# Performance work log

Hardware: AMD Instinct MI355X
Metric: run time of the kernel (lower is better)

Reference implementation:

```python
import jax, jax.numpy as jnp
import numpy as np

EPS = 1e-8  # LayerNorm eps from __init__
B, C1, T, H, AUX, OUT = 4, 512, 256, 64, 256, 512


def prelu(x, a):
    # torch nn.PReLU with num_parameters=1 (scalar slope, init 0.25)
    return jnp.where(x >= 0, x, a * x)


def layernorm(x, w, b):
    mu = jnp.mean(x, axis=-1, keepdims=True)
    var = jnp.mean(jnp.square(x - mu), axis=-1, keepdims=True)
    return (x - mu) * jax.lax.rsqrt(var + EPS) * w + b


def setup_inputs() -> dict:
    key = jax.random.key(0)
    k0, k1, k2, k3 = jax.random.split(key, 4)
    x = jax.random.normal(k0, (B, C1, T, H), dtype=jnp.float32)
    s = jax.random.normal(k1, (B, AUX), dtype=jnp.float32)
    # pre: PReLU + LayerNorm(input_dim)
    prelu1_a = jnp.full((), 0.25, dtype=jnp.float32)
    ln1_w = jnp.ones((C1,), dtype=jnp.float32)
    ln1_b = jnp.zeros((C1,), dtype=jnp.float32)
    # post: Linear(input_dim+aux_dim, output_dim) + PReLU + LayerNorm(output_dim)
    lim = 1.0 / np.sqrt(C1 + AUX)
    W = jax.random.uniform(k2, (OUT, C1 + AUX), jnp.float32, -lim, lim)
    b = jax.random.uniform(k3, (OUT,), jnp.float32, -lim, lim)
    prelu2_a = jnp.full((), 0.25, dtype=jnp.float32)
    ln2_w = jnp.ones((OUT,), dtype=jnp.float32)
    ln2_b = jnp.zeros((OUT,), dtype=jnp.float32)
    return {"x": x, "s": s, "prelu1_a": prelu1_a, "ln1_w": ln1_w, "ln1_b": ln1_b,
            "W": W, "b": b, "prelu2_a": prelu2_a, "ln2_w": ln2_w, "ln2_b": ln2_b}


def reference(x, s, prelu1_a, ln1_w, ln1_b, W, b, prelu2_a, ln2_w, ln2_b):
    Bb, C, Tt, Hh = x.shape
    xt = jnp.transpose(x, (0, 2, 3, 1))  # b c t h -> b t h c
    # NOTE: source computes pre(x) into y but then overwrites y with the concat,
    # so this branch is dead code; reproduced for fidelity (DCE'd under jit).
    _pre = layernorm(prelu(xt, prelu1_a), ln1_w, ln1_b)
    # speaker embedding broadcast over (t, h), concatenated on channel axis
    s4 = jnp.broadcast_to(s[:, None, None, :], (Bb, Tt, Hh, s.shape[-1]))
    cat = jnp.concatenate([xt, s4], axis=-1)            # (b, t, h, c1+aux)
    z = jnp.einsum('bthc,oc->btho', cat, W) + b          # Linear
    z = layernorm(prelu(z, prelu2_a), ln2_w, ln2_b)      # PReLU + LayerNorm
    y = xt + z                                           # residual add
    return jnp.transpose(y, (0, 3, 1, 2))                # b t h c -> b c t h
```

## Files before the change

### kernel.cpp

```cpp
#include <hip/hip_runtime.h>
#include <hip/hip_bf16.h>

#define B_   4
#define C1_  512
#define T_   256
#define H_   64
#define TH_  (T_*H_)
#define AUX_ 256
#define OUT_ 512
#define INF_ 768
#define BK   32
#define THB  64
#define WSTR 40

typedef __attribute__((ext_vector_type(8))) short bf16x8;
typedef __attribute__((ext_vector_type(4))) float f32x4;

__device__ __forceinline__ ushort bf16u(float f) {
    __hip_bfloat16 h = __float2bfloat16(f);
    return *reinterpret_cast<ushort*>(&h);
}

__global__ void wconv_kernel(const float* __restrict__ W, ushort* __restrict__ Wbf) {
    int idx = (blockIdx.x * 256 + threadIdx.x) * 4;
    int o = idx >> 9, c = idx & 511;
    const float4 v = *(const float4*)(W + (size_t)o * INF_ + c);
    ushort4 u = make_ushort4(bf16u(v.x), bf16u(v.y), bf16u(v.z), bf16u(v.w));
    *(ushort4*)(Wbf + idx) = u;
}

__global__ void sw_kernel(const float* __restrict__ s, const float* __restrict__ W,
                          const float* __restrict__ bias, float* __restrict__ sW) {
    __shared__ float sl[AUX_];
    int b = blockIdx.x, o = threadIdx.x;
    for (int c = threadIdx.x; c < AUX_; c += 512) sl[c] = s[b * AUX_ + c];
    __syncthreads();
    float acc = bias[o];
    const float* wr = W + (size_t)o * INF_ + C1_;
    #pragma unroll 8
    for (int c = 0; c < AUX_; c += 4) {
        float4 w = *(const float4*)(wr + c);
        acc += sl[c] * w.x + sl[c+1] * w.y + sl[c+2] * w.z + sl[c+3] * w.w;
    }
    sW[b * OUT_ + o] = acc;
}

__global__ __launch_bounds__(512) void fused_kernel(
    const float* __restrict__ X, const ushort* __restrict__ Wbf,
    const float* __restrict__ sW, const float* __restrict__ a2p,
    const float* __restrict__ ln2w, const float* __restrict__ ln2b,
    float* __restrict__ Yout)
{
    __shared__ __align__(16) ushort Ws[C1_ * WSTR];
    __shared__ __align__(16) ushort Xs[THB * WSTR];
    __shared__ float red[8][THB][2];

    const int tid  = threadIdx.x;
    const int lane = tid & 63;
    const int w    = tid >> 6;
    const int b    = blockIdx.y;
    const int th0  = blockIdx.x * THB;
    const float* xb = X + (size_t)b * C1_ * TH_;

    const int l15 = lane & 15;
    const int lhi = lane >> 4;

    f32x4 acc[4][4] = {};

    for (int kk = 0; kk < C1_ / BK; ++kk) {
        const int kc = kk * BK;
        #pragma unroll
        for (int it = 0; it < 4; ++it) {
            int slot = tid + it * 512;
            int r = slot >> 2, q = slot & 3;
            const uint4 v = *(const uint4*)(Wbf + (size_t)r * C1_ + kc + q * 8);
            *(uint4*)(&Ws[r * WSTR + q * 8]) = v;
        }
        {
            int i = tid >> 4, j4 = tid & 15;
            const float4 v = *(const float4*)(xb + (size_t)(kc + i) * TH_ + th0 + j4 * 4);
            Xs[(j4 * 4 + 0) * WSTR + i] = bf16u(v.x);
            Xs[(j4 * 4 + 1) * WSTR + i] = bf16u(v.y);
            Xs[(j4 * 4 + 2) * WSTR + i] = bf16u(v.z);
            Xs[(j4 * 4 + 3) * WSTR + i] = bf16u(v.w);
        }
        __syncthreads();
        bf16x8 af[4], bfr[4];
        #pragma unroll
        for (int fm = 0; fm < 4; ++fm)
            af[fm] = *(const bf16x8*)(&Ws[(w * 64 + fm * 16 + l15) * WSTR + lhi * 8]);
        #pragma unroll
        for (int fn = 0; fn < 4; ++fn)
            bfr[fn] = *(const bf16x8*)(&Xs[(fn * 16 + l15) * WSTR + lhi * 8]);
        #pragma unroll
        for (int fm = 0; fm < 4; ++fm) {
            #pragma unroll
            for (int fn = 0; fn < 4; ++fn)
                acc[fm][fn] = __builtin_amdgcn_mfma_f32_16x16x32_bf16(
                    af[fm], bfr[fn], acc[fm][fn], 0, 0, 0);
        }
        __syncthreads();
    }

    const float a2 = a2p[0];
    const int obase = w * 64;
    float swv[4][4];
    #pragma unroll
    for (int fm = 0; fm < 4; ++fm)
        #pragma unroll
        for (int r = 0; r < 4; ++r)
            swv[fm][r] = sW[b * OUT_ + obase + fm * 16 + lhi * 4 + r];

    float s1[4] = {0,0,0,0}, s2[4] = {0,0,0,0};
    #pragma unroll
    for (int fm = 0; fm < 4; ++fm) {
        #pragma unroll
        for (int fn = 0; fn < 4; ++fn) {
            #pragma unroll
            for (int r = 0; r < 4; ++r) {
                float z = acc[fm][fn][r] + swv[fm][r];
                float v = z >= 0.f ? z : a2 * z;
                acc[fm][fn][r] = v;
                s1[fn] += v; s2[fn] += v * v;
            }
        }
    }
    #pragma unroll
    for (int fn = 0; fn < 4; ++fn) {
        s1[fn] += __shfl_xor(s1[fn], 16, 64);
        s2[fn] += __shfl_xor(s2[fn], 16, 64);
        s1[fn] += __shfl_xor(s1[fn], 32, 64);
        s2[fn] += __shfl_xor(s2[fn], 32, 64);
    }
    if (lane < 16) {
        #pragma unroll
        for (int fn = 0; fn < 4; ++fn) {
            red[w][fn * 16 + lane][0] = s1[fn];
            red[w][fn * 16 + lane][1] = s2[fn];
        }
    }
    __syncthreads();
    float mean[4], rstd[4];
    #pragma unroll
    for (int fn = 0; fn < 4; ++fn) {
        float t1 = 0.f, t2 = 0.f;
        #pragma unroll
        for (int ww = 0; ww < 8; ++ww) {
            t1 += red[ww][fn * 16 + l15][0];
            t2 += red[ww][fn * 16 + l15][1];
        }
        float mu = t1 * (1.0f / OUT_);
        mean[fn] = mu;
        float var = t2 * (1.0f / OUT_) - mu * mu;
        rstd[fn] = rsqrtf(var + 1e-8f);
    }
    #pragma unroll
    for (int fm = 0; fm < 4; ++fm) {
        #pragma unroll
        for (int r = 0; r < 4; ++r) {
            int o = obase + fm * 16 + lhi * 4 + r;
            float wo = ln2w[o], bo = ln2b[o];
            const float* xrow = xb + (size_t)o * TH_ + th0;
            float* yrow = Yout + ((size_t)b * OUT_ + o) * TH_ + th0;
            #pragma unroll
            for (int fn = 0; fn < 4; ++fn) {
                int col = fn * 16 + l15;
                float resid = xrow[col];
                yrow[col] = resid + (acc[fm][fn][r] - mean[fn]) * rstd[fn] * wo + bo;
            }
        }
    }
}

extern "C" void kernel_launch(void* const* d_in, const int* in_sizes, int n_in,
                              void* d_out, int out_size, void* d_ws, size_t ws_size,
                              hipStream_t stream) {
    const float* x    = (const float*)d_in[0];
    const float* s    = (const float*)d_in[1];
    const float* W    = (const float*)d_in[5];
    const float* bias = (const float*)d_in[6];
    const float* a2   = (const float*)d_in[7];
    const float* ln2w = (const float*)d_in[8];
    const float* ln2b = (const float*)d_in[9];
    float* out = (float*)d_out;

    ushort* Wbf = (ushort*)d_ws;
    float*  sW  = (float*)((char*)d_ws + C1_ * OUT_ * 2);

    wconv_kernel<<<256, 256, 0, stream>>>(W, Wbf);
    sw_kernel<<<B_, 512, 0, stream>>>(s, W, bias, sW);
    dim3 grid(TH_ / THB, B_);
    fused_kernel<<<grid, 512, 0, stream>>>(x, Wbf, sW, a2, ln2w, ln2b, out);
}
```

Baseline: 352.0 us.

## Double-buffer GEMM tiles with direct global-to-LDS loads and XOR swizzle

The K-loop now uses two LDS buffers so the next W tile and X tile are fetched while MFMAs run on the current one. W tiles are loaded with global_load_lds straight into shared memory, and an XOR swizzle replaces row padding to avoid bank conflicts. X is prefetched into registers, then converted and written to the other buffer after the MFMAs, which leaves one barrier per iteration. LDS use roughly doubles, and the launch bound asks for 4 waves per SIMD, which may cap registers and cause spills.

```diff
diff --git a/kernel.cpp b/kernel.cpp
--- a/kernel.cpp
+++ b/kernel.cpp
@@ -11,10 +11,12 @@
 #define INF_ 768
 #define BK   32
 #define THB  64
-#define WSTR 40
+#define NKS  (C1_/BK)
 
 typedef __attribute__((ext_vector_type(8))) short bf16x8;
 typedef __attribute__((ext_vector_type(4))) float f32x4;
+typedef __attribute__((address_space(3))) void* lds_vp;
+typedef const __attribute__((address_space(1))) void* gbl_vp;
 
 __device__ __forceinline__ ushort bf16u(float f) {
     __hip_bfloat16 h = __float2bfloat16(f);
@@ -45,14 +47,14 @@
     sW[b * OUT_ + o] = acc;
 }
 
-__global__ __launch_bounds__(512) void fused_kernel(
+__global__ __launch_bounds__(512, 4) void fused_kernel(
     const float* __restrict__ X, const ushort* __restrict__ Wbf,
     const float* __restrict__ sW, const float* __restrict__ a2p,
     const float* __restrict__ ln2w, const float* __restrict__ ln2b,
     float* __restrict__ Yout)
 {
-    __shared__ __align__(16) ushort Ws[C1_ * WSTR];
-    __shared__ __align__(16) ushort Xs[THB * WSTR];
+    __shared__ __align__(16) ushort Ws[2][C1_ * BK];
+    __shared__ __align__(16) ushort Xs[2][THB * BK];
     __shared__ float red[8][THB][2];
 
     const int tid  = threadIdx.x;
@@ -61,44 +63,74 @@
     const int b    = blockIdx.y;
     const int th0  = blockIdx.x * THB;
     const float* xb = X + (size_t)b * C1_ * TH_;
-
     const int l15 = lane & 15;
     const int lhi = lane >> 4;
 
+    const int xcol = tid & 63;
+    const int xg   = tid >> 6;
+    float xr[8];
+
     f32x4 acc[4][4] = {};
 
-    for (int kk = 0; kk < C1_ / BK; ++kk) {
-        const int kc = kk * BK;
-        #pragma unroll
-        for (int it = 0; it < 4; ++it) {
-            int slot = tid + it * 512;
-            int r = slot >> 2, q = slot & 3;
-            const uint4 v = *(const uint4*)(Wbf + (size_t)r * C1_ + kc + q * 8);
-            *(uint4*)(&Ws[r * WSTR + q * 8]) = v;
-        }
-        {
-            int i = tid >> 4, j4 = tid & 15;
-            const float4 v = *(const float4*)(xb + (size_t)(kc + i) * TH_ + th0 + j4 * 4);
-            Xs[(j4 * 4 + 0) * WSTR + i] = bf16u(v.x);
-            Xs[(j4 * 4 + 1) * WSTR + i] = bf16u(v.y);
-            Xs[(j4 * 4 + 2) * WSTR + i] = bf16u(v.z);
-            Xs[(j4 * 4 + 3) * WSTR + i] = bf16u(v.w);
-        }
-        __syncthreads();
+    auto stage_w = [&](int buf, int kc) {
+        #pragma unroll
+        for (int i = 0; i < 4; ++i) {
+            int row  = i * 128 + (tid >> 2);
+            int slot = tid & 3;
+            int cch  = slot ^ ((row >> 1) & 3);
+            const ushort* g = Wbf + (size_t)row * C1_ + kc + cch * 8;
+            __builtin_amdgcn_global_load_lds((gbl_vp)g,
+                (lds_vp)&Ws[buf][i * 4096 + tid * 8], 16, 0, 0);
+        }
+    };
+    auto xload = [&](int kc) {
+        if (tid < 256) {
+            #pragma unroll
+            for (int j = 0; j < 8; ++j)
+                xr[j] = xb[(size_t)(kc + xg * 8 + j) * TH_ + th0 + xcol];
+        }
+    };
+    auto xwrite = [&](int buf) {
+        if (tid < 256) {
+            int slot = xg ^ ((xcol >> 1) & 3);
+            bf16x8 v;
+            #pragma unroll
+            for (int j = 0; j < 8; ++j) v[j] = (short)bf16u(xr[j]);
+            *(bf16x8*)&Xs[buf][xcol * BK + slot * 8] = v;
+        }
+    };
+
+    stage_w(0, 0);
+    xload(0);
+    xwrite(0);
+    __syncthreads();
+
+    for (int kk = 0; kk < NKS; ++kk) {
+        const int cur = kk & 1;
+        if (kk + 1 < NKS) {
+            stage_w(cur ^ 1, (kk + 1) * BK);
+            xload((kk + 1) * BK);
+        }
         bf16x8 af[4], bfr[4];
         #pragma unroll
+        for (int fm = 0; fm < 4; ++fm) {
+            int row  = w * 64 + fm * 16 + l15;
+            int slot = lhi ^ ((row >> 1) & 3);
+            af[fm] = *(const bf16x8*)&Ws[cur][row * BK + slot * 8];
+        }
+        #pragma unroll
+        for (int fn = 0; fn < 4; ++fn) {
+            int row  = fn * 16 + l15;
+            int slot = lhi ^ ((row >> 1) & 3);
+            bfr[fn] = *(const bf16x8*)&Xs[cur][row * BK + slot * 8];
+        }
+        #pragma unroll
         for (int fm = 0; fm < 4; ++fm)
-            af[fm] = *(const bf16x8*)(&Ws[(w * 64 + fm * 16 + l15) * WSTR + lhi * 8]);
-        #pragma unroll
-        for (int fn = 0; fn < 4; ++fn)
-            bfr[fn] = *(const bf16x8*)(&Xs[(fn * 16 + l15) * WSTR + lhi * 8]);
-        #pragma unroll
-        for (int fm = 0; fm < 4; ++fm) {
             #pragma unroll
             for (int fn = 0; fn < 4; ++fn)
                 acc[fm][fn] = __builtin_amdgcn_mfma_f32_16x16x32_bf16(
                     af[fm], bfr[fn], acc[fm][fn], 0, 0, 0);
-        }
+        if (kk + 1 < NKS) xwrite(cur ^ 1);
         __syncthreads();
     }
 
```

Measured after the change: 521.6 us. 1.48x slower.
